# Kernel optimization log

Hardware: AMD Instinct MI355X
Metric: run time of the kernel (lower is better)

The kernel has to match this reference:

```python
import jax, jax.numpy as jnp
import numpy as np

B, T, D = 2, 2048, 1024
H, DH = 16, 64
WINDOW = 256
SCALE = DH ** -0.5


def setup_inputs() -> dict:
    key = jax.random.key(0)
    ks = jax.random.split(key, 5)
    x = jax.random.normal(ks[0], (B, T, D), dtype=jnp.float32)
    # Linear params (y = x @ W + b form)
    w_qkv = jax.random.normal(ks[1], (D, 3 * D), dtype=jnp.float32) * (D ** -0.5)
    b_qkv = jnp.zeros((3 * D,), dtype=jnp.float32)
    w_out = jax.random.normal(ks[2], (D, D), dtype=jnp.float32) * (D ** -0.5)
    b_out = jnp.zeros((D,), dtype=jnp.float32)
    return {"x": x, "w_qkv": w_qkv, "b_qkv": b_qkv, "w_out": w_out, "b_out": b_out}


def reference(x, w_qkv, b_qkv, w_out, b_out):
    Bs, Ts, Ds = x.shape
    qkv = x @ w_qkv + b_qkv  # [B,T,3D]
    q, k, v = jnp.split(qkv, 3, axis=-1)
    # [B,H,T,dh]
    def heads(t):
        return t.reshape(Bs, Ts, H, DH).transpose(0, 2, 1, 3)
    q, k, v = heads(q), heads(k), heads(v)
    scores = jnp.einsum('bhqd,bhkd->bhqk', q, k) * SCALE
    i = jnp.arange(Ts)[:, None]
    j = jnp.arange(Ts)[None, :]
    # allowed: i - WINDOW <= j <= i  (causal + local window)
    allowed = (j <= i) & (j >= i - WINDOW)
    scores = jnp.where(allowed, scores, -jnp.inf)
    attn = jax.nn.softmax(scores, axis=-1)  # dropout is identity in eval
    out = jnp.einsum('bhqk,bhkd->bhqd', attn, v)
    out = out.transpose(0, 2, 1, 3).reshape(Bs, Ts, Ds)
    return out @ w_out + b_out
```

## Files before the change

kernel.cpp:

```cpp
#include <hip/hip_runtime.h>

#define BN 2
#define T_DIM 2048
#define D_DIM 1024
#define H_N 16
#define DH_N 64
#define WIN 256
#define NROWS (BN * T_DIM)
#define KDIM 1024

typedef __attribute__((ext_vector_type(8))) short bf16x8;
typedef __attribute__((ext_vector_type(4))) float f32x4;
typedef __attribute__((ext_vector_type(8))) unsigned short ushort8;
typedef __attribute__((ext_vector_type(4))) unsigned short u16x4;

static __device__ __forceinline__ unsigned short f2bf(float f) {
  unsigned int u = __float_as_uint(f);
  unsigned int r = (u + 0x7FFFu + ((u >> 16) & 1u)) >> 16;
  return (unsigned short)r;
}

static __device__ __forceinline__ void gl_lds16(const void* g, void* l) {
  __builtin_amdgcn_global_load_lds(
      (const __attribute__((address_space(1))) unsigned int*)g,
      (__attribute__((address_space(3))) unsigned int*)l, 16, 0, 0);
}

#define MFMA16(a, b, c) __builtin_amdgcn_mfma_f32_16x16x32_bf16(a, b, c, 0, 0, 0)

static __device__ __forceinline__ void transpose_tile(
    const float* __restrict__ src, unsigned short* __restrict__ dst, int R,
    int C, int bx, int by, float* tile ) {
  const int t = threadIdx.x;
  const int bc = bx * 64, br = by * 64;
#pragma unroll
  for (int i = 0; i < 16; ++i) {
    int idx = i * 256 + t;
    int r = idx >> 6, c = idx & 63;
    tile[r * 65 + c] = src[(size_t)(br + r) * C + bc + c];
  }
  __syncthreads();
#pragma unroll
  for (int i = 0; i < 16; ++i) {
    int idx = i * 256 + t;
    int r = idx >> 6, c = idx & 63;
    dst[(size_t)(bc + r) * R + br + c] = f2bf(tile[c * 65 + r]);
  }
}

__global__ __launch_bounds__(256) void convert_all(
    const float* __restrict__ x, const float* __restrict__ w_qkv,
    const float* __restrict__ w_out, unsigned short* __restrict__ xbf,
    unsigned short* __restrict__ wqkvt, unsigned short* __restrict__ woutt) {
  __shared__ float tile[64 * 65];
  const int id = blockIdx.x;
  if (id < 2048) {
    int i = (id * 256 + threadIdx.x) * 8;
    float4 a = *(const float4*)(x + i);
    float4 b = *(const float4*)(x + i + 4);
    ushort8 o;
    o[0] = f2bf(a.x); o[1] = f2bf(a.y); o[2] = f2bf(a.z); o[3] = f2bf(a.w);
    o[4] = f2bf(b.x); o[5] = f2bf(b.y); o[6] = f2bf(b.z); o[7] = f2bf(b.w);
    *(ushort8*)(xbf + i) = o;
  } else if (id < 2816) {
    int j = id - 2048;
    transpose_tile(w_qkv, wqkvt, D_DIM, 3 * D_DIM, j % 48, j / 48, tile);
  } else {
    int j = id - 2816;
    transpose_tile(w_out, woutt, D_DIM, D_DIM, j % 16, j / 16, tile);
  }
}

__global__ __launch_bounds__(512) void gemm_qkv_8p(
    const unsigned short* __restrict__ A, const unsigned short* __restrict__ Bt,
    const float* __restrict__ bias, unsigned short* __restrict__ qo,
    unsigned short* __restrict__ ko, unsigned short* __restrict__ vto) {
  __shared__ unsigned short As[2][256 * 64];
  __shared__ unsigned short Bs[2][192 * 64];

  const int tid = threadIdx.x;
  const int w = tid >> 6, l = tid & 63;
  const int wr = w >> 2, wc = w & 3;
  const int l15 = l & 15, kslc = l >> 4;

  const int id = blockIdx.x;
  const int wg = (id & 7) * 32 + (id >> 3);
  const int bx = wg & 15, by = wg >> 4;
  const int r0 = by * 256, c0 = bx * 192;

  const unsigned short* Ag = A + (size_t)r0 * KDIM;
  const unsigned short* Bg = Bt + (size_t)c0 * KDIM;

  f32x4 acc[8][3];
#pragma unroll
  for (int i = 0; i < 8; ++i)
#pragma unroll
    for (int j = 0; j < 3; ++j) acc[i][j] = (f32x4){0.f, 0.f, 0.f, 0.f};

  const int grow = tid >> 3;
  const int gcol = (tid & 7) ^ (grow & 7);

#define STAGE_A(T, BUF, CH)                                                    \
  gl_lds16(Ag + (size_t)((CH)*64 + grow) * KDIM + (T)*64 + gcol * 8,           \
           (char*)&As[BUF][0] + (CH)*8192 + w * 1024)
#define STAGE_B(T, BUF, CH)                                                    \
  gl_lds16(Bg + (size_t)((CH)*64 + grow) * KDIM + (T)*64 + gcol * 8,           \
           (char*)&Bs[BUF][0] + (CH)*8192 + w * 1024)

#define LDA(CB, mi, ks)                                                        \
  (*(const bf16x8*)((const char*)&As[CB][0] +                                  \
                    (wr * 128 + (mi)*16 + l15) * 128 +                         \
                    ((((ks)*4 + kslc) ^ (l15 & 7)) << 4)))
#define LDB(CB, ni, ks)                                                        \
  (*(const bf16x8*)((const char*)&Bs[CB][0] +                                  \
                    (wc * 48 + (ni)*16 + l15) * 128 +                          \
                    ((((ks)*4 + kslc) ^ (l15 & 7)) << 4)))

#define CLUSTER12(B_, A0, A1, A2, A3, B0, B1, B2)                              \
  do {                                                                         \
    __builtin_amdgcn_s_setprio(1);                                             \
    acc[B_ + 0][0] = MFMA16(A0, B0, acc[B_ + 0][0]);                           \
    acc[B_ + 0][1] = MFMA16(A0, B1, acc[B_ + 0][1]);                           \
    acc[B_ + 0][2] = MFMA16(A0, B2, acc[B_ + 0][2]);                           \
    acc[B_ + 1][0] = MFMA16(A1, B0, acc[B_ + 1][0]);                           \
    acc[B_ + 1][1] = MFMA16(A1, B1, acc[B_ + 1][1]);                           \
    acc[B_ + 1][2] = MFMA16(A1, B2, acc[B_ + 1][2]);                           \
    acc[B_ + 2][0] = MFMA16(A2, B0, acc[B_ + 2][0]);                           \
    acc[B_ + 2][1] = MFMA16(A2, B1, acc[B_ + 2][1]);                           \
    acc[B_ + 2][2] = MFMA16(A2, B2, acc[B_ + 2][2]);                           \
    acc[B_ + 3][0] = MFMA16(A3, B0, acc[B_ + 3][0]);                           \
    acc[B_ + 3][1] = MFMA16(A3, B1, acc[B_ + 3][1]);                           \
    acc[B_ + 3][2] = MFMA16(A3, B2, acc[B_ + 3][2]);                           \
    __builtin_amdgcn_s_setprio(0);                                             \
  } while (0)

  STAGE_A(0, 0, 0); STAGE_A(0, 0, 1); STAGE_A(0, 0, 2); STAGE_A(0, 0, 3);
  STAGE_B(0, 0, 0); STAGE_B(0, 0, 1); STAGE_B(0, 0, 2);

#pragma unroll 1
  for (int t = 0; t < 15; ++t) {
    const int cb = t & 1, nb = cb ^ 1;
    STAGE_A(t + 1, nb, 0); STAGE_A(t + 1, nb, 1);
    asm volatile("s_waitcnt vmcnt(2)" ::: "memory");
    __builtin_amdgcn_s_barrier();
    {
      bf16x8 a0 = LDA(cb, 0, 0), a1 = LDA(cb, 1, 0), a2 = LDA(cb, 2, 0),
             a3 = LDA(cb, 3, 0);
      bf16x8 b0 = LDB(cb, 0, 0), b1 = LDB(cb, 1, 0), b2 = LDB(cb, 2, 0);
      CLUSTER12(0, a0, a1, a2, a3, b0, b1, b2);
      __builtin_amdgcn_s_barrier();
      bf16x8 a4 = LDA(cb, 4, 0), a5 = LDA(cb, 5, 0), a6 = LDA(cb, 6, 0),
             a7 = LDA(cb, 7, 0);
      STAGE_A(t + 1, nb, 2); STAGE_A(t + 1, nb, 3);
      __builtin_amdgcn_s_barrier();
      CLUSTER12(4, a4, a5, a6, a7, b0, b1, b2);
      __builtin_amdgcn_s_barrier();
      bf16x8 c0_ = LDA(cb, 0, 1), c1_ = LDA(cb, 1, 1), c2_ = LDA(cb, 2, 1),
             c3_ = LDA(cb, 3, 1);
      bf16x8 d0 = LDB(cb, 0, 1), d1 = LDB(cb, 1, 1), d2 = LDB(cb, 2, 1);
      STAGE_B(t + 1, nb, 0); STAGE_B(t + 1, nb, 1);
      __builtin_amdgcn_s_barrier();
      CLUSTER12(0, c0_, c1_, c2_, c3_, d0, d1, d2);
      __builtin_amdgcn_s_barrier();
      bf16x8 c4 = LDA(cb, 4, 1), c5 = LDA(cb, 5, 1), c6 = LDA(cb, 6, 1),
             c7 = LDA(cb, 7, 1);
      STAGE_B(t + 1, nb, 2);
      __builtin_amdgcn_s_barrier();
      CLUSTER12(4, c4, c5, c6, c7, d0, d1, d2);
      __builtin_amdgcn_s_barrier();
    }
  }
  asm volatile("s_waitcnt vmcnt(0)" ::: "memory");
  __builtin_amdgcn_s_barrier();
  {
    bf16x8 a0 = LDA(1, 0, 0), a1 = LDA(1, 1, 0), a2 = LDA(1, 2, 0),
           a3 = LDA(1, 3, 0);
    bf16x8 b0 = LDB(1, 0, 0), b1 = LDB(1, 1, 0), b2 = LDB(1, 2, 0);
    CLUSTER12(0, a0, a1, a2, a3, b0, b1, b2);
    bf16x8 a4 = LDA(1, 4, 0), a5 = LDA(1, 5, 0), a6 = LDA(1, 6, 0),
           a7 = LDA(1, 7, 0);
    CLUSTER12(4, a4, a5, a6, a7, b0, b1, b2);
    bf16x8 c0_ = LDA(1, 0, 1), c1_ = LDA(1, 1, 1), c2_ = LDA(1, 2, 1),
           c3_ = LDA(1, 3, 1);
    bf16x8 d0 = LDB(1, 0, 1), d1 = LDB(1, 1, 1), d2 = LDB(1, 2, 1);
    CLUSTER12(0, c0_, c1_, c2_, c3_, d0, d1, d2);
    bf16x8 c4 = LDA(1, 4, 1), c5 = LDA(1, 5, 1), c6 = LDA(1, 6, 1),
           c7 = LDA(1, 7, 1);
    CLUSTER12(4, c4, c5, c6, c7, d0, d1, d2);
  }
#undef STAGE_A
#undef STAGE_B
#undef LDA
#undef LDB
#undef CLUSTER12

#pragma unroll
  for (int ni = 0; ni < 3; ++ni) {
    const int col0 = c0 + wc * 48 + ni * 16;
    const int which = col0 >> 10;
    const int h = (col0 >> 6) & 15;
    const int dh = (col0 & 63) + l15;
    const float bv = bias[col0 + l15];
#pragma unroll
    for (int mi = 0; mi < 8; ++mi) {
      int row = r0 + wr * 128 + mi * 16 + (l >> 4) * 4;
      int b_ = row >> 11, t0 = row & 2047;
      if (which == 2) {
        u16x4 pk;
#pragma unroll
        for (int j = 0; j < 4; ++j) pk[j] = f2bf(acc[mi][ni][j] + bv);
        *(u16x4*)(vto + ((size_t)(b_ * H_N + h) * DH_N + dh) * T_DIM + t0) = pk;
      } else {
        float mul = (which == 0) ? 0.125f : 1.0f;
        unsigned short* dst = (which == 0) ? qo : ko;
#pragma unroll
        for (int j = 0; j < 4; ++j)
          dst[((size_t)(b_ * H_N + h) * T_DIM + t0 + j) * DH_N + dh] =
              f2bf((acc[mi][ni][j] + bv) * mul);
      }
    }
  }
}

__global__ __launch_bounds__(256) void gemm_out_p4(
    const unsigned short* __restrict__ A, const unsigned short* __restrict__ Bt,
    const float* __restrict__ bias, float* __restrict__ fo) {
  __shared__ unsigned short As[4][4096];
  __shared__ unsigned short Bs[4][4096];

  const int tid = threadIdx.x;
  const int w = tid >> 6, l = tid & 63;
  const int wr = w >> 1, wc = w & 1;
  const int l15 = l & 15, kslc = l >> 4;

  const int id = blockIdx.x;
  const int wg = (id & 7) * 32 + (id >> 3);
  const int bx = wg & 7, by = wg >> 3;
  const int r0 = by * 128, c0 = bx * 128;

  const unsigned short* Ag = A + (size_t)r0 * KDIM;
  const unsigned short* Bg = Bt + (size_t)c0 * KDIM;

  f32x4 acc[4][4];
#pragma unroll
  for (int i = 0; i < 4; ++i)
#pragma unroll
    for (int j = 0; j < 4; ++j) acc[i][j] = (f32x4){0.f, 0.f, 0.f, 0.f};

  const int srow = l >> 2;
  const int srcslot = (l & 3) ^ ((l >> 3) & 3);

#define STAGE_O(T, BUF)                                                        \
  do {                                                                         \
    const size_t kk0 = (size_t)(T) * 32;                                       \
    gl_lds16(Ag + (size_t)(w * 16 + srow) * KDIM + kk0 + srcslot * 8,          \
             (char*)&As[BUF][0] + w * 1024);                                   \
    gl_lds16(Ag + (size_t)(64 + w * 16 + srow) * KDIM + kk0 + srcslot * 8,     \
             (char*)&As[BUF][0] + (4 + w) * 1024);                             \
    gl_lds16(Bg + (size_t)(w * 16 + srow) * KDIM + kk0 + srcslot * 8,          \
             (char*)&Bs[BUF][0] + w * 1024);                                   \
    gl_lds16(Bg + (size_t)(64 + w * 16 + srow) * KDIM + kk0 + srcslot * 8,     \
             (char*)&Bs[BUF][0] + (4 + w) * 1024);                             \
  } while (0)

#define OCOMPUTE(CB)                                                           \
  do {                                                                         \
    bf16x8 af[4], bfr[4];                                                      \
    _Pragma("unroll") for (int mi = 0; mi < 4; ++mi) {                         \
      int row = wr * 64 + mi * 16 + l15;                                       \
      af[mi] = *(const bf16x8*)((const char*)&As[CB][0] + row * 64 +           \
                                ((kslc ^ ((row >> 1) & 3)) << 4));             \
    }                                                                          \
    _Pragma("unroll") for (int ni = 0; ni < 4; ++ni) {                         \
      int row = wc * 64 + ni * 16 + l15;                                       \
      bfr[ni] = *(const bf16x8*)((const char*)&Bs[CB][0] + row * 64 +          \
                                 ((kslc ^ ((row >> 1) & 3)) << 4));            \
    }                                                                          \
    __builtin_amdgcn_s_setprio(1);                                             \
    _Pragma("unroll") for (int mi = 0; mi < 4; ++mi)                           \
        _Pragma("unroll") for (int ni = 0; ni < 4; ++ni) acc[mi][ni] =         \
            MFMA16(af[mi], bfr[ni], acc[mi][ni]);                              \
    __builtin_amdgcn_s_setprio(0);                                             \
  } while (0)

  STAGE_O(0, 0);
  STAGE_O(1, 1);

  for (int t = 0; t < 30; ++t) {
    STAGE_O(t + 2, (t + 2) & 3);
    asm volatile("s_waitcnt vmcnt(8)" ::: "memory");
    __builtin_amdgcn_s_barrier();
    OCOMPUTE(t & 3);
  }
  asm volatile("s_waitcnt vmcnt(4)" ::: "memory");
  __builtin_amdgcn_s_barrier();
  OCOMPUTE(2);
  asm volatile("s_waitcnt vmcnt(0)" ::: "memory");
  __builtin_amdgcn_s_barrier();
  OCOMPUTE(3);
#undef STAGE_O
#undef OCOMPUTE

#pragma unroll
  for (int mi = 0; mi < 4; ++mi) {
#pragma unroll
    for (int ni = 0; ni < 4; ++ni) {
      int row = r0 + wr * 64 + mi * 16 + (l >> 4) * 4;
      int col = c0 + wc * 64 + ni * 16 + l15;
      float bv = bias[col];
#pragma unroll
      for (int j = 0; j < 4; ++j)
        fo[(size_t)(row + j) * D_DIM + col] = acc[mi][ni][j] + bv;
    }
  }
}

__global__ __launch_bounds__(256) void attn_direct(
    const unsigned short* __restrict__ qbf,
    const unsigned short* __restrict__ kbf,
    const unsigned short* __restrict__ vtbf,
    unsigned short* __restrict__ ctx) {
  const int tid = threadIdx.x;
  const int w = tid >> 6, l = tid & 63;
  const int g = l >> 4, ln = l & 15;

  const int bid = blockIdx.x;
  const int r_ = bid >> 3;
  const int bh = (bid & 7) * 4 + (r_ & 3);
  const int qt = r_ >> 2;
  const int q0 = qt * 64;
  const int q_abs = q0 + w * 16 + ln;

  const unsigned short* kp = kbf + (size_t)bh * T_DIM * DH_N;
  const unsigned short* vtp = vtbf + (size_t)bh * DH_N * T_DIM;

  bf16x8 qf0, qf1;
  {
    const unsigned short* qp = qbf + ((size_t)bh * T_DIM + q_abs) * DH_N;
    qf0 = *(const bf16x8*)(qp + g * 8);
    qf1 = *(const bf16x8*)(qp + 32 + g * 8);
  }

#define KAP(row) \
  (32 * (((row) >> 4) & 1) + 8 * (((row)&15) >> 2) + 4 * ((row) >> 5) + ((row)&3))
  const unsigned short* kbase[4];
#pragma unroll
  for (int nk = 0; nk < 4; ++nk) {
    int rrow = nk * 16 + ln;
    kbase[nk] = kp + (size_t)KAP(rrow) * DH_N + g * 8;
  }
  const unsigned short* vbase[4];
#pragma unroll
  for (int nd = 0; nd < 4; ++nd)
    vbase[nd] = vtp + (size_t)(nd * 16 + ln) * T_DIM + g * 8;
#undef KAP

  f32x4 acc_o[4];
#pragma unroll
  for (int nd = 0; nd < 4; ++nd) acc_o[nd] = (f32x4){0.f, 0.f, 0.f, 0.f};
  float m = -1e30f, lsum = 0.f;

  const int kt_lo = (q0 >= WIN) ? (q0 - WIN) : 0;
  for (int kt = kt_lo; kt <= q0; kt += 64) {
    f32x4 sacc[4];
#pragma unroll
    for (int nk = 0; nk < 4; ++nk) sacc[nk] = (f32x4){0.f, 0.f, 0.f, 0.f};
#pragma unroll
    for (int ks = 0; ks < 2; ++ks) {
      bf16x8 qf = ks ? qf1 : qf0;
#pragma unroll
      for (int nk = 0; nk < 4; ++nk) {
        bf16x8 kf = *(const bf16x8*)(kbase[nk] + (size_t)kt * DH_N + ks * 32);
        sacc[nk] = MFMA16(kf, qf, sacc[nk]);
      }
    }

    float p[4][4];
    float tm = -1e30f;
#pragma unroll
    for (int nk = 0; nk < 4; ++nk)
#pragma unroll
      for (int j = 0; j < 4; ++j) {
        int k_abs = kt + 32 * (nk & 1) + 8 * g + 4 * (nk >> 1) + j;
        float s = sacc[nk][j];
        bool ok = (k_abs <= q_abs) && (k_abs + WIN >= q_abs);
        s = ok ? s : -1e30f;
        p[nk][j] = s;
        tm = fmaxf(tm, s);
      }
    tm = fmaxf(tm, __shfl_xor(tm, 16, 64));
    tm = fmaxf(tm, __shfl_xor(tm, 32, 64));
    float mn = fmaxf(m, tm);
    float sc = __expf(m - mn);
    float ps = 0.f;
#pragma unroll
    for (int nk = 0; nk < 4; ++nk)
#pragma unroll
      for (int j = 0; j < 4; ++j) {
        p[nk][j] = __expf(p[nk][j] - mn);
        ps += p[nk][j];
      }
    ps += __shfl_xor(ps, 16, 64);
    ps += __shfl_xor(ps, 32, 64);
    lsum = lsum * sc + ps;
    m = mn;
#pragma unroll
    for (int nd = 0; nd < 4; ++nd) {
      acc_o[nd][0] *= sc; acc_o[nd][1] *= sc;
      acc_o[nd][2] *= sc; acc_o[nd][3] *= sc;
    }

    unsigned int pk[4][2];
#pragma unroll
    for (int nk = 0; nk < 4; ++nk) {
      pk[nk][0] = (unsigned)f2bf(p[nk][0]) | ((unsigned)f2bf(p[nk][1]) << 16);
      pk[nk][1] = (unsigned)f2bf(p[nk][2]) | ((unsigned)f2bf(p[nk][3]) << 16);
    }

#pragma unroll
    for (int ks = 0; ks < 2; ++ks) {
      union { unsigned int d[4]; bf16x8 v; } pf;
      pf.d[0] = pk[ks][0];     pf.d[1] = pk[ks][1];
      pf.d[2] = pk[2 + ks][0]; pf.d[3] = pk[2 + ks][1];
#pragma unroll
      for (int nd = 0; nd < 4; ++nd) {
        bf16x8 vf = *(const bf16x8*)(vbase[nd] + kt + ks * 32);
        acc_o[nd] = MFMA16(vf, pf.v, acc_o[nd]);
      }
    }
  }

  float inv = 1.f / lsum;
  const int b_ = bh >> 4, h = bh & 15;
  unsigned short* op = ctx + ((size_t)b_ * T_DIM + q_abs) * D_DIM + h * DH_N;
#pragma unroll
  for (int nd = 0; nd < 4; ++nd) {
    u16x4 o;
#pragma unroll
    for (int j = 0; j < 4; ++j) o[j] = f2bf(acc_o[nd][j] * inv);
    *(u16x4*)(op + nd * 16 + g * 4) = o;
  }
}

extern "C" void kernel_launch(void* const* d_in, const int* in_sizes, int n_in,
                              void* d_out, int out_size, void* d_ws,
                              size_t ws_size, hipStream_t stream) {
  const float* x = (const float*)d_in[0];
  const float* w_qkv = (const float*)d_in[1];
  const float* b_qkv = (const float*)d_in[2];
  const float* w_out = (const float*)d_in[3];
  const float* b_out = (const float*)d_in[4];
  float* out = (float*)d_out;

  const size_t per = (size_t)BN * H_N * T_DIM * DH_N;
  unsigned short* qbf = (unsigned short*)d_ws;
  unsigned short* kbf = qbf + per;
  unsigned short* vtbf = kbf + per;
  unsigned short* xbf = vtbf + per;
  unsigned short* wqkvt = xbf + (size_t)NROWS * D_DIM;
  unsigned short* woutt = wqkvt + (size_t)3 * D_DIM * D_DIM;
  unsigned short* ctxbf = woutt + (size_t)D_DIM * D_DIM;

  convert_all<<<dim3(3072), dim3(256), 0, stream>>>(x, w_qkv, w_out, xbf,
                                                    wqkvt, woutt);

  gemm_qkv_8p<<<dim3(256), dim3(512), 0, stream>>>(xbf, wqkvt, b_qkv, qbf, kbf,
                                                   vtbf);

  attn_direct<<<dim3(BN * H_N * (T_DIM / 64)), dim3(256), 0, stream>>>(
      qbf, kbf, vtbf, ctxbf);

  gemm_out_p4<<<dim3(256), dim3(256), 0, stream>>>(ctxbf, woutt, b_out, out);
}
```

Before: 109.4 us.

## Process two query sub-tiles per wave in attention, use exp2 and skip interior masks

The attention kernel now has each wave handle 32 queries as two independent 16-row sub-tiles. Each K and V fragment load feeds two MFMAs, and the two online-softmax chains can interleave for more instruction-level parallelism. The grid shrinks to 512 blocks of 128 queries. Q is pre-scaled by log2(e)/8 so the kernel can use exp2f, and masking runs only on the boundary tiles. The risks are higher register pressure, fewer blocks for occupancy, and an extra partly masked key tile per wave because the 64-aligned key range no longer matches each wave's 32-query offset.

```diff
diff --git a/kernel.cpp b/kernel.cpp
--- a/kernel.cpp
+++ b/kernel.cpp
@@ -211,7 +211,7 @@
         for (int j = 0; j < 4; ++j) pk[j] = f2bf(acc[mi][ni][j] + bv);
         *(u16x4*)(vto + ((size_t)(b_ * H_N + h) * DH_N + dh) * T_DIM + t0) = pk;
       } else {
-        float mul = (which == 0) ? 0.125f : 1.0f;
+        float mul = (which == 0) ? 0.18033688f : 1.0f;
         unsigned short* dst = (which == 0) ? qo : ko;
 #pragma unroll
         for (int j = 0; j < 4; ++j)
@@ -315,7 +315,7 @@
   }
 }
 
-__global__ __launch_bounds__(256) void attn_direct(
+__global__ __launch_bounds__(256) void attn_ilp2(
     const unsigned short* __restrict__ qbf,
     const unsigned short* __restrict__ kbf,
     const unsigned short* __restrict__ vtbf,
@@ -325,20 +325,23 @@
   const int g = l >> 4, ln = l & 15;
 
   const int bid = blockIdx.x;
-  const int r_ = bid >> 3;
-  const int bh = (bid & 7) * 4 + (r_ & 3);
-  const int qt = r_ >> 2;
-  const int q0 = qt * 64;
-  const int q_abs = q0 + w * 16 + ln;
+  const int bh = (bid & 7) * 4 + ((bid >> 3) & 3);
+  const int qt = bid >> 5;
+  const int qw0 = qt * 128 + w * 32;
+  const int qA = qw0 + ln;
+  const int qB = qw0 + 16 + ln;
 
   const unsigned short* kp = kbf + (size_t)bh * T_DIM * DH_N;
   const unsigned short* vtp = vtbf + (size_t)bh * DH_N * T_DIM;
 
-  bf16x8 qf0, qf1;
+  bf16x8 qfA0, qfA1, qfB0, qfB1;
   {
-    const unsigned short* qp = qbf + ((size_t)bh * T_DIM + q_abs) * DH_N;
-    qf0 = *(const bf16x8*)(qp + g * 8);
-    qf1 = *(const bf16x8*)(qp + 32 + g * 8);
+    const unsigned short* qpA = qbf + ((size_t)bh * T_DIM + qA) * DH_N;
+    qfA0 = *(const bf16x8*)(qpA + g * 8);
+    qfA1 = *(const bf16x8*)(qpA + 32 + g * 8);
+    const unsigned short* qpB = qbf + ((size_t)bh * T_DIM + qB) * DH_N;
+    qfB0 = *(const bf16x8*)(qpB + g * 8);
+    qfB1 = *(const bf16x8*)(qpB + 32 + g * 8);
   }
 
 #define KAP(row) \
@@ -355,90 +358,132 @@
     vbase[nd] = vtp + (size_t)(nd * 16 + ln) * T_DIM + g * 8;
 #undef KAP
 
-  f32x4 acc_o[4];
-#pragma unroll
-  for (int nd = 0; nd < 4; ++nd) acc_o[nd] = (f32x4){0.f, 0.f, 0.f, 0.f};
-  float m = -1e30f, lsum = 0.f;
-
-  const int kt_lo = (q0 >= WIN) ? (q0 - WIN) : 0;
-  for (int kt = kt_lo; kt <= q0; kt += 64) {
-    f32x4 sacc[4];
-#pragma unroll
-    for (int nk = 0; nk < 4; ++nk) sacc[nk] = (f32x4){0.f, 0.f, 0.f, 0.f};
-#pragma unroll
-    for (int ks = 0; ks < 2; ++ks) {
-      bf16x8 qf = ks ? qf1 : qf0;
-#pragma unroll
-      for (int nk = 0; nk < 4; ++nk) {
-        bf16x8 kf = *(const bf16x8*)(kbase[nk] + (size_t)kt * DH_N + ks * 32);
-        sacc[nk] = MFMA16(kf, qf, sacc[nk]);
-      }
+  f32x4 accA[4], accB[4];
+#pragma unroll
+  for (int nd = 0; nd < 4; ++nd) {
+    accA[nd] = (f32x4){0.f, 0.f, 0.f, 0.f};
+    accB[nd] = (f32x4){0.f, 0.f, 0.f, 0.f};
+  }
+  float mA = -1e30f, lsA = 0.f, mB = -1e30f, lsB = 0.f;
+
+  const int ktl = (qw0 >= WIN) ? ((qw0 - WIN) & ~63) : 0;
+  const int kth = qw0 & ~63;
+
+#define MASK_MAX(S, P, TM, QABS, KT, MASKED)                                   \
+  do {                                                                         \
+    _Pragma("unroll") for (int nk = 0; nk < 4; ++nk)                           \
+        _Pragma("unroll") for (int j = 0; j < 4; ++j) {                        \
+      float s_ = S[nk][j];                                                     \
+      if (MASKED) {                                                            \
+        int k_abs = (KT) + 32 * (nk & 1) + 8 * g + 4 * (nk >> 1) + j;          \
+        bool ok = (k_abs <= (QABS)) && (k_abs + WIN >= (QABS));                \
+        s_ = ok ? s_ : -1e30f;                                                 \
+      }                                                                        \
+      P[nk][j] = s_;                                                           \
+    }                                                                          \
+    float a0 = fmaxf(P[0][0], P[0][1]), a1 = fmaxf(P[0][2], P[0][3]);          \
+    float a2 = fmaxf(P[1][0], P[1][1]), a3 = fmaxf(P[1][2], P[1][3]);          \
+    float a4 = fmaxf(P[2][0], P[2][1]), a5 = fmaxf(P[2][2], P[2][3]);          \
+    float a6 = fmaxf(P[3][0], P[3][1]), a7 = fmaxf(P[3][2], P[3][3]);          \
+    TM = fmaxf(fmaxf(fmaxf(a0, a1), fmaxf(a2, a3)),                            \
+               fmaxf(fmaxf(a4, a5), fmaxf(a6, a7)));                           \
+    TM = fmaxf(TM, __shfl_xor(TM, 16, 64));                                    \
+    TM = fmaxf(TM, __shfl_xor(TM, 32, 64));                                    \
+  } while (0)
+
+#define ONLINE(P, TM, M, LS, ACC, PK)                                          \
+  do {                                                                         \
+    float mn = fmaxf(M, TM);                                                   \
+    float sc = exp2f(M - mn);                                                  \
+    _Pragma("unroll") for (int nk = 0; nk < 4; ++nk)                           \
+        _Pragma("unroll") for (int j = 0; j < 4; ++j)                          \
+            P[nk][j] = exp2f(P[nk][j] - mn);                                   \
+    float s0 = (P[0][0] + P[0][1]) + (P[0][2] + P[0][3]);                      \
+    float s1 = (P[1][0] + P[1][1]) + (P[1][2] + P[1][3]);                      \
+    float s2 = (P[2][0] + P[2][1]) + (P[2][2] + P[2][3]);                      \
+    float s3 = (P[3][0] + P[3][1]) + (P[3][2] + P[3][3]);                      \
+    float ps = (s0 + s1) + (s2 + s3);                                          \
+    ps += __shfl_xor(ps, 16, 64);                                              \
+    ps += __shfl_xor(ps, 32, 64);                                              \
+    LS = LS * sc + ps;                                                         \
+    M = mn;                                                                    \
+    _Pragma("unroll") for (int nd = 0; nd < 4; ++nd) {                         \
+      ACC[nd][0] *= sc; ACC[nd][1] *= sc; ACC[nd][2] *= sc; ACC[nd][3] *= sc;  \
+    }                                                                          \
+    _Pragma("unroll") for (int nk = 0; nk < 4; ++nk) {                         \
+      PK[nk][0] = (unsigned)f2bf(P[nk][0]) | ((unsigned)f2bf(P[nk][1]) << 16); \
+      PK[nk][1] = (unsigned)f2bf(P[nk][2]) | ((unsigned)f2bf(P[nk][3]) << 16); \
+    }                                                                          \
+  } while (0)
+
+#define TILE_BODY(KT, MASKED)                                                  \
+  do {                                                                         \
+    f32x4 sA[4], sB[4];                                                        \
+    _Pragma("unroll") for (int nk = 0; nk < 4; ++nk) {                         \
+      sA[nk] = (f32x4){0.f, 0.f, 0.f, 0.f};                                    \
+      sB[nk] = (f32x4){0.f, 0.f, 0.f, 0.f};                                    \
+    }                                                                          \
+    _Pragma("unroll") for (int ks = 0; ks < 2; ++ks) {                         \
+      bf16x8 qa = ks ? qfA1 : qfA0;                                            \
+      bf16x8 qb = ks ? qfB1 : qfB0;                                            \
+      _Pragma("unroll") for (int nk = 0; nk < 4; ++nk) {                       \
+        bf16x8 kf = *(const bf16x8*)(kbase[nk] + (size_t)(KT)*DH_N + ks * 32); \
+        sA[nk] = MFMA16(kf, qa, sA[nk]);                                       \
+        sB[nk] = MFMA16(kf, qb, sB[nk]);                                       \
+      }                                                                        \
+    }                                                                          \
+    float pA[4][4], pB[4][4];                                                  \
+    float tmA, tmB;                                                            \
+    MASK_MAX(sA, pA, tmA, qA, KT, MASKED);                                     \
+    MASK_MAX(sB, pB, tmB, qB, KT, MASKED);                                     \
+    unsigned int pkA[4][2], pkB[4][2];                                         \
+    ONLINE(pA, tmA, mA, lsA, accA, pkA);                                       \
+    ONLINE(pB, tmB, mB, lsB, accB, pkB);                                       \
+    _Pragma("unroll") for (int ks = 0; ks < 2; ++ks) {                         \
+      union { unsigned int d[4]; bf16x8 v; } pfA, pfB;                         \
+      pfA.d[0] = pkA[ks][0];     pfA.d[1] = pkA[ks][1];                        \
+      pfA.d[2] = pkA[2 + ks][0]; pfA.d[3] = pkA[2 + ks][1];                    \
+      pfB.d[0] = pkB[ks][0];     pfB.d[1] = pkB[ks][1];                        \
+      pfB.d[2] = pkB[2 + ks][0]; pfB.d[3] = pkB[2 + ks][1];                    \
+      _Pragma("unroll") for (int nd = 0; nd < 4; ++nd) {                       \
+        bf16x8 vf = *(const bf16x8*)(vbase[nd] + (KT) + ks * 32);              \
+        accA[nd] = MFMA16(vf, pfA.v, accA[nd]);                                \
+        accB[nd] = MFMA16(vf, pfB.v, accB[nd]);                                \
+      }                                                                        \
+    }                                                                          \
+  } while (0)
+
+  for (int kt = ktl; kt <= kth; kt += 64) {
+    const bool masked = (kt == kth) || (qw0 >= WIN && kt == ktl);
+    if (masked) TILE_BODY(kt, 1);
+    else        TILE_BODY(kt, 0);
+  }
+#undef TILE_BODY
+#undef ONLINE
+#undef MASK_MAX
+
+  const int b_ = bh >> 4, h = bh & 15;
+  {
+    float inv = 1.f / lsA;
+    unsigned short* op = ctx + ((size_t)b_ * T_DIM + qA) * D_DIM + h * DH_N;
+#pragma unroll
+    for (int nd = 0; nd < 4; ++nd) {
+      u16x4 o;
+#pragma unroll
+      for (int j = 0; j < 4; ++j) o[j] = f2bf(accA[nd][j] * inv);
+      *(u16x4*)(op + nd * 16 + g * 4) = o;
     }
-
-    float p[4][4];
-    float tm = -1e30f;
-#pragma unroll
-    for (int nk = 0; nk < 4; ++nk)
-#pragma unroll
-      for (int j = 0; j < 4; ++j) {
-        int k_abs = kt + 32 * (nk & 1) + 8 * g + 4 * (nk >> 1) + j;
-        float s = sacc[nk][j];
-        bool ok = (k_abs <= q_abs) && (k_abs + WIN >= q_abs);
-        s = ok ? s : -1e30f;
-        p[nk][j] = s;
-        tm = fmaxf(tm, s);
-      }
-    tm = fmaxf(tm, __shfl_xor(tm, 16, 64));
-    tm = fmaxf(tm, __shfl_xor(tm, 32, 64));
-    float mn = fmaxf(m, tm);
-    float sc = __expf(m - mn);
-    float ps = 0.f;
-#pragma unroll
-    for (int nk = 0; nk < 4; ++nk)
-#pragma unroll
-      for (int j = 0; j < 4; ++j) {
-        p[nk][j] = __expf(p[nk][j] - mn);
-        ps += p[nk][j];
-      }
-    ps += __shfl_xor(ps, 16, 64);
-    ps += __shfl_xor(ps, 32, 64);
-    lsum = lsum * sc + ps;
-    m = mn;
+  }
+  {
+    float inv = 1.f / lsB;
+    unsigned short* op = ctx + ((size_t)b_ * T_DIM + qB) * D_DIM + h * DH_N;
 #pragma unroll
     for (int nd = 0; nd < 4; ++nd) {
-      acc_o[nd][0] *= sc; acc_o[nd][1] *= sc;
-      acc_o[nd][2] *= sc; acc_o[nd][3] *= sc;
+      u16x4 o;
+#pragma unroll
+      for (int j = 0; j < 4; ++j) o[j] = f2bf(accB[nd][j] * inv);
+      *(u16x4*)(op + nd * 16 + g * 4) = o;
     }
-
-    unsigned int pk[4][2];
-#pragma unroll
-    for (int nk = 0; nk < 4; ++nk) {
-      pk[nk][0] = (unsigned)f2bf(p[nk][0]) | ((unsigned)f2bf(p[nk][1]) << 16);
-      pk[nk][1] = (unsigned)f2bf(p[nk][2]) | ((unsigned)f2bf(p[nk][3]) << 16);
-    }
-
-#pragma unroll
-    for (int ks = 0; ks < 2; ++ks) {
-      union { unsigned int d[4]; bf16x8 v; } pf;
-      pf.d[0] = pk[ks][0];     pf.d[1] = pk[ks][1];
-      pf.d[2] = pk[2 + ks][0]; pf.d[3] = pk[2 + ks][1];
-#pragma unroll
-      for (int nd = 0; nd < 4; ++nd) {
-        bf16x8 vf = *(const bf16x8*)(vbase[nd] + kt + ks * 32);
-        acc_o[nd] = MFMA16(vf, pf.v, acc_o[nd]);
-      }
-    }
-  }
-
-  float inv = 1.f / lsum;
-  const int b_ = bh >> 4, h = bh & 15;
-  unsigned short* op = ctx + ((size_t)b_ * T_DIM + q_abs) * D_DIM + h * DH_N;
-#pragma unroll
-  for (int nd = 0; nd < 4; ++nd) {
-    u16x4 o;
-#pragma unroll
-    for (int j = 0; j < 4; ++j) o[j] = f2bf(acc_o[nd][j] * inv);
-    *(u16x4*)(op + nd * 16 + g * 4) = o;
   }
 }
 
@@ -467,8 +512,7 @@
   gemm_qkv_8p<<<dim3(256), dim3(512), 0, stream>>>(xbf, wqkvt, b_qkv, qbf, kbf,
                                                    vtbf);
 
-  attn_direct<<<dim3(BN * H_N * (T_DIM / 64)), dim3(256), 0, stream>>>(
-      qbf, kbf, vtbf, ctxbf);
+  attn_ilp2<<<dim3(512), dim3(256), 0, stream>>>(qbf, kbf, vtbf, ctxbf);
 
   gemm_out_p4<<<dim3(256), dim3(256), 0, stream>>>(ctxbf, woutt, b_out, out);
 }
```

After: 94.02 us. -14.0%, faster.
